# Optimization experiments

Measured on AMD Instinct MI355X. Metric: run time of the kernel, lower is better.

The kernel has to match this reference:

```python
import math
import jax, jax.numpy as jnp
import numpy as np

B, FIN, FOUT, M = 8192, 512, 512, 8
INV_SQRT_2PI = 1.0 / math.sqrt(2.0 * math.pi)
SQRT_HALF = math.sqrt(0.5)


def setup_inputs() -> dict:
    key = jax.random.key(0)
    k = jax.random.split(key, 7)
    x = jax.random.normal(k[0], (B, FIN), dtype=jnp.float32)
    nan_mask = jax.random.uniform(k[1], (B, FIN)) < 0.15
    nan_mask = nan_mask.at[:, 0].set(True)  # every row has >=1 NaN -> GMM path taken, den > 0
    x = jnp.where(nan_mask, jnp.nan, x)
    bound = 1.0 / math.sqrt(FIN)  # torch nn.Linear default init range
    W = jax.random.uniform(k[2], (FOUT, FIN), dtype=jnp.float32, minval=-bound, maxval=bound)
    b = jax.random.uniform(k[3], (FOUT,), dtype=jnp.float32, minval=-bound, maxval=bound)
    mean_p = 0.1 * jax.random.normal(k[4], (M, FIN), dtype=jnp.float32)
    log_std2 = 0.1 * jax.random.normal(k[5], (M, FIN), dtype=jnp.float32)
    log_weights = jax.random.normal(k[6], (M,), dtype=jnp.float32)
    return {"x": x, "W": W, "b": b, "mean_p": mean_p,
            "log_std2": log_std2, "log_weights": log_weights}


def _nr(z):
    # pdf(z) + z * Phi(z), the Gaussian 'nr' function from the paper
    pdf = INV_SQRT_2PI * jnp.exp(-0.5 * z * z)
    return pdf + z * 0.5 * (1.0 + jax.lax.erf(z * SQRT_HALF))


def reference(x, W, b, mean_p, log_std2, log_weights):
    nan = jnp.isnan(x)                         # [B, FIN]
    empty = jnp.any(nan, axis=-1)[:, None]     # [B, 1]
    mask = nan[:, None, :]                     # [B, 1, FIN]
    # impute NaNs with per-mode GMM means
    mean = jnp.where(mask, mean_p, x[:, None, :])                   # [B, M, FIN]
    num = jnp.einsum('bmf,of->bom', mean, W) + b[None, :, None]     # [B, FOUT, M]
    std2 = jnp.where(mask, jnp.exp(log_std2), jnp.float32(0.0))     # [B, M, FIN]
    den = jnp.sqrt(jnp.einsum('bmf,of->bom', std2, W * W))          # [B, FOUT, M]
    nr = den * _nr(num / (den + 1e-9))                              # [B, FOUT, M]
    mixture = nr @ jax.nn.softmax(log_weights)                      # [B, FOUT]
    return jnp.where(empty, mixture, jax.nn.relu(num[..., 0]))
```

## Files before the change

kernel.cpp:

```cpp
#include <hip/hip_runtime.h>
#include <math.h>

typedef __attribute__((ext_vector_type(8))) short short8;
typedef __attribute__((ext_vector_type(8))) _Float16 f16x8;
typedef __attribute__((ext_vector_type(4))) float floatx4;
typedef __attribute__((ext_vector_type(4))) int intx4;
typedef __attribute__((ext_vector_type(16))) int intx16;

#define B_ROWS 8192
#define FIN    512
#define FOUT   512
#define QS     4096.0f
#define QINV   0.000244140625f

#define WSB_SW   0UL
#define WSB_CNT  64UL
#define WSB_BASE 65536UL
#define WSB_XCH  16842752UL
#define WSB_MSK  25231360UL
#define WSB_WH   33619968UL
#define WSB_BCT  34144256UL

__device__ __forceinline__ void gl2lds16(const void* g, void* l) {
    __builtin_amdgcn_global_load_lds((const __attribute__((address_space(1))) void*)g,
                                     (__attribute__((address_space(3))) void*)l,
                                     16, 0, 0);
}

__device__ __forceinline__ float frcp(float x) { float r; asm("v_rcp_f32 %0, %1" : "=v"(r) : "v"(x)); return r; }
__device__ __forceinline__ float frsq(float x) { float r; asm("v_rsq_f32 %0, %1" : "=v"(r) : "v"(x)); return r; }
__device__ __forceinline__ float fexp2(float x){ float r; asm("v_exp_f32 %0, %1" : "=v"(r) : "v"(x)); return r; }

__global__ __launch_bounds__(256) void prep_all(const float* __restrict__ W,
                                                const float* __restrict__ mean_p,
                                                const float* __restrict__ ls2,
                                                const float* __restrict__ x,
                                                const float* __restrict__ lw,
                                                signed char* __restrict__ bct,
                                                _Float16* __restrict__ Wh,
                                                _Float16* __restrict__ xch,
                                                signed char* __restrict__ msk,
                                                int* __restrict__ cnts,
                                                float* __restrict__ wsf) {
    int tid = threadIdx.x, lane = tid & 63, wid = tid >> 6;
    if (blockIdx.x < 2048) {
        int n  = blockIdx.x * 4 + wid;
        int fc = lane << 3;
        int o = n >> 4, t = n & 15;
        const float* wp = W + (size_t)o * FIN + fc;
        float v[8];
        if (t < 8) {
            const float* mp = mean_p + (size_t)t * FIN + fc;
#pragma unroll
            for (int j = 0; j < 8; ++j) v[j] = mp[j] * wp[j];
            if (t == 0) {
                f16x8 wv;
#pragma unroll
                for (int j = 0; j < 8; ++j) wv[j] = (_Float16)wp[j];
                *(f16x8*)(Wh + (size_t)o * FIN + fc) = wv;
            }
        } else {
            const float* lp = ls2 + (size_t)(t - 8) * FIN + fc;
#pragma unroll
            for (int j = 0; j < 8; ++j) v[j] = expf(lp[j]) * wp[j] * wp[j];
        }
        unsigned long long pack = 0;
#pragma unroll
        for (int j = 0; j < 8; ++j) {
            int q = (int)rintf(v[j] * QS);
            q = q > 127 ? 127 : (q < -127 ? -127 : q);
            pack |= ((unsigned long long)(unsigned char)(signed char)q) << (8 * j);
        }
        *(unsigned long long*)(bct + (size_t)n * FIN + fc) = pack;
    } else {
        int row = (blockIdx.x - 2048) * 4 + wid;
        const float* xr = x + (size_t)row * FIN + lane * 8;
        float4 a = *(const float4*)xr;
        float4 b = *(const float4*)(xr + 4);
        float v[8] = {a.x, a.y, a.z, a.w, b.x, b.y, b.z, b.w};
        f16x8 xo;
        unsigned long long mpack = 0;
        bool anyn = false;
#pragma unroll
        for (int j = 0; j < 8; ++j) {
            bool isn = (v[j] != v[j]);
            anyn |= isn;
            xo[j] = (_Float16)(isn ? 0.f : v[j]);
            mpack |= ((unsigned long long)(isn ? 1u : 0u)) << (8 * j);
        }
        *(f16x8*)(xch + (size_t)row * FIN + lane * 8) = xo;
        *(unsigned long long*)(msk + (size_t)row * FIN + lane * 8) = mpack;
        bool any = __any(anyn);
        if (lane == 0) cnts[row] = any ? 1 : 0;
        if (blockIdx.x == 2048 && tid == 0) {
            float mx = lw[0];
            for (int m = 1; m < 8; ++m) mx = fmaxf(mx, lw[m]);
            float e[8]; float s = 0.f;
            for (int m = 0; m < 8; ++m) { e[m] = expf(lw[m] - mx); s += e[m]; }
            for (int m = 0; m < 8; ++m) wsf[m] = e[m] / s;
        }
    }
}

__global__ __launch_bounds__(256) void gemm_base(const _Float16* __restrict__ xch,
                                                 const _Float16* __restrict__ Wh,
                                                 _Float16* __restrict__ base) {
    __shared__ short As[128 * 64];
    __shared__ short Bs[64 * 64];
    int tid = threadIdx.x, lane = tid & 63, wid = tid >> 6;
    int wr = wid >> 1, wc = wid & 1;
    int bb0 = blockIdx.y * 128;
    int ob0 = blockIdx.x * 64;

    floatx4 acc[4][2];
#pragma unroll
    for (int mi = 0; mi < 4; ++mi)
#pragma unroll
        for (int ni = 0; ni < 2; ++ni) acc[mi][ni] = (floatx4){0.f, 0.f, 0.f, 0.f};

    for (int ks = 0; ks < FIN; ks += 64) {
        __syncthreads();
#pragma unroll
        for (int i = 0; i < 4; ++i) {
            int cid = i * 256 + tid, row = cid >> 3, c = cid & 7;
            short8 v = *(const short8*)((const short*)xch + (((size_t)(bb0 + row)) << 9) + ks + c * 8);
            *(short8*)(&As[row * 64 + ((c ^ (row & 7)) << 3)]) = v;
        }
#pragma unroll
        for (int i = 0; i < 2; ++i) {
            int cid = i * 256 + tid, row = cid >> 3, c = cid & 7;
            short8 v = *(const short8*)((const short*)Wh + (((size_t)(ob0 + row)) << 9) + ks + c * 8);
            *(short8*)(&Bs[row * 64 + ((c ^ (row & 7)) << 3)]) = v;
        }
        __syncthreads();
#pragma unroll
        for (int kk = 0; kk < 2; ++kk) {
            f16x8 av[4], bv[2];
#pragma unroll
            for (int mi = 0; mi < 4; ++mi) {
                int row = wr * 64 + mi * 16 + (lane & 15);
                int c = kk * 4 + (lane >> 4);
                av[mi] = *(const f16x8*)(&As[row * 64 + ((c ^ (row & 7)) << 3)]);
            }
#pragma unroll
            for (int ni = 0; ni < 2; ++ni) {
                int row = wc * 32 + ni * 16 + (lane & 15);
                int c = kk * 4 + (lane >> 4);
                bv[ni] = *(const f16x8*)(&Bs[row * 64 + ((c ^ (row & 7)) << 3)]);
            }
#pragma unroll
            for (int mi = 0; mi < 4; ++mi)
#pragma unroll
                for (int ni = 0; ni < 2; ++ni)
                    acc[mi][ni] = __builtin_amdgcn_mfma_f32_16x16x32_f16(av[mi], bv[ni], acc[mi][ni], 0, 0, 0);
        }
    }
#pragma unroll
    for (int mi = 0; mi < 4; ++mi)
#pragma unroll
        for (int ni = 0; ni < 2; ++ni)
#pragma unroll
            for (int r = 0; r < 4; ++r) {
                int row = bb0 + wr * 64 + mi * 16 + (lane >> 4) * 4 + r;
                int col = ob0 + wc * 32 + ni * 16 + (lane & 15);
                base[(size_t)row * FOUT + col] = (_Float16)acc[mi][ni][r];
            }
}

__global__ __launch_bounds__(512, 4) void gmm_fused(const signed char* __restrict__ msk,
                                                    const signed char* __restrict__ bct,
                                                    const float* __restrict__ wsf,
                                                    const int* __restrict__ cnts,
                                                    const _Float16* __restrict__ baseh,
                                                    const float* __restrict__ bias,
                                                    float* __restrict__ out) {
    __shared__ char lds[73728];

    int tid = threadIdx.x, lane = tid & 63, wid = tid >> 6;
    int wr = wid >> 1, wc = wid & 1;

    int id = blockIdx.x, gid = id >> 6, wi = id & 63;
    int my = (gid >> 3) * 8 + (wi >> 3);
    int nx = (gid & 7) * 8 + (wi & 7);
    int b0 = my * 256, n0 = nx * 128;

    const char* mB = (const char*)msk;
    const char* bB = (const char*)bct;

    int rA0 = (wid + 0) * 16 + (lane >> 2);
    int rA1 = (wid + 8) * 16 + (lane >> 2);
    int rB0 = rA0;
    const char* gA0 = mB + (size_t)(b0 + rA0) * 512 + (((lane & 3) ^ ((rA0 >> 1) & 3)) << 4);
    const char* gA1 = mB + (size_t)(b0 + rA1) * 512 + (((lane & 3) ^ ((rA1 >> 1) & 3)) << 4);
    const char* gB0 = bB + (size_t)(n0 + rB0) * 512 + (((lane & 3) ^ ((rB0 >> 1) & 3)) << 4);
    const int lA0o = (wid + 0) * 1024;
    const int lA1o = (wid + 8) * 1024;
    const int lB0o = 16384 + wid * 1024;

    int offA[2], offB[2];
#pragma unroll
    for (int mi = 0; mi < 2; ++mi) {
        int r = wr * 64 + mi * 32 + (lane & 31);
        offA[mi] = r * 64 + ((((lane >> 5) ^ ((r >> 1) & 3))) << 4);
    }
#pragma unroll
    for (int ni = 0; ni < 2; ++ni) {
        int r = wc * 64 + ni * 32 + (lane & 31);
        offB[ni] = 16384 + r * 64 + ((((lane >> 5) ^ ((r >> 1) & 3))) << 4);
    }

    intx16 acc[2][2];
#pragma unroll
    for (int mi = 0; mi < 2; ++mi)
#pragma unroll
        for (int ni = 0; ni < 2; ++ni)
#pragma unroll
            for (int e = 0; e < 16; ++e) acc[mi][ni][e] = 0;

#define STAGE(T)                                             \
    {                                                        \
        const int bo_ = ((T) % 3) * 24576;                   \
        gl2lds16(gA0 + (T) * 64, lds + bo_ + lA0o);          \
        gl2lds16(gA1 + (T) * 64, lds + bo_ + lA1o);          \
        gl2lds16(gB0 + (T) * 64, lds + bo_ + lB0o);          \
    }

    STAGE(0); STAGE(1);

#pragma unroll
    for (int t = 0; t < 8; ++t) {
        if (t < 7) asm volatile("s_waitcnt vmcnt(3)" ::: "memory");
        else       asm volatile("s_waitcnt vmcnt(0)" ::: "memory");
        __builtin_amdgcn_s_barrier();
        asm volatile("" ::: "memory");
        if (t + 2 < 8) STAGE(t + 2);

        const int bo = (t % 3) * 24576;
#pragma unroll
        for (int kk = 0; kk < 2; ++kk) {
            const int kx = kk << 5;
            intx4 av[2], bv[2];
#pragma unroll
            for (int mi = 0; mi < 2; ++mi) av[mi] = *(const intx4*)(lds + bo + (offA[mi] ^ kx));
#pragma unroll
            for (int ni = 0; ni < 2; ++ni) bv[ni] = *(const intx4*)(lds + bo + (offB[ni] ^ kx));
            __builtin_amdgcn_s_setprio(1);
#pragma unroll
            for (int mi = 0; mi < 2; ++mi)
#pragma unroll
                for (int ni = 0; ni < 2; ++ni)
                    acc[mi][ni] = __builtin_amdgcn_mfma_i32_32x32x32_i8(av[mi], bv[ni], acc[mi][ni], 0, 0, 0);
            __builtin_amdgcn_s_setprio(0);
        }
    }
#undef STAGE

    __syncthreads();

    float swv[8];
#pragma unroll
    for (int m = 0; m < 8; ++m) swv[m] = wsf[m];

    int* sci = (int*)lds + wid * 1056;
    int cl = lane & 31, oh = lane >> 5;

#pragma unroll
    for (int mi = 0; mi < 2; ++mi) {
#pragma unroll
        for (int ni = 0; ni < 2; ++ni) {
#pragma unroll
            for (int reg = 0; reg < 16; ++reg) {
                int r = (reg & 3) + 8 * (reg >> 2) + 4 * oh;
                sci[r * 33 + cl] = acc[mi][ni][reg];
            }
            __asm__ volatile("s_waitcnt lgkmcnt(0)" ::: "memory");

            float cn[8], cd[8];
#pragma unroll
            for (int tt = 0; tt < 8; ++tt) cn[tt] = (float)sci[cl * 33 + oh * 16 + tt] * QINV;
#pragma unroll
            for (int tt = 0; tt < 8; ++tt) cd[tt] = (float)sci[cl * 33 + oh * 16 + 8 + tt] * QINV;

            int b = b0 + wr * 64 + mi * 32 + cl;
            int o = ((n0 + wc * 64 + ni * 32) >> 4) + oh;
            float basev = (float)baseh[(size_t)b * FOUT + o];
            float K0 = basev + bias[o];
            bool empty = cnts[b] > 0;

            float mix = 0.f, num0 = 0.f;
#pragma unroll
            for (int m = 0; m < 8; ++m) {
                float num = K0 + cn[m];
                if (m == 0) num0 = num;
                float rs  = frsq(fmaxf(cd[m], 1e-20f));
                float den = cd[m] * rs;
                float z   = num * rs;
                float az  = fabsf(z);
                float E   = fexp2((z * z) * -0.72134752044448170f);
                float t1  = frcp(fmaf(0.2316419f, az, 1.0f));
                float h   = fmaf(t1, 0.5307027145f, -0.7265760135f);
                h = fmaf(t1, h, 0.7107068705f);
                h = fmaf(t1, h, -0.142248368f);
                h = fmaf(t1, h, 0.127414796f);
                float u   = t1 * h;
                float v   = fmaf(-az, u, 0.3989422804014327f);
                float g   = fmaf(E, v, fmaxf(z, 0.f));
                mix = fmaf(swv[m], den * g, mix);
            }
            out[(size_t)b * FOUT + o] = empty ? mix : fmaxf(num0, 0.f);
        }
    }
}

extern "C" void kernel_launch(void* const* d_in, const int* in_sizes, int n_in,
                              void* d_out, int out_size, void* d_ws, size_t ws_size,
                              hipStream_t stream) {
    const float* x        = (const float*)d_in[0];
    const float* W        = (const float*)d_in[1];
    const float* bvec     = (const float*)d_in[2];
    const float* mean_p   = (const float*)d_in[3];
    const float* log_std2 = (const float*)d_in[4];
    const float* lw       = (const float*)d_in[5];
    float* out = (float*)d_out;

    char* wsb = (char*)d_ws;
    float*        wsf  = (float*)wsb;
    int*          cnts = (int*)(wsb + WSB_CNT);
    _Float16*     base = (_Float16*)(wsb + WSB_BASE);
    _Float16*     xch  = (_Float16*)(wsb + WSB_XCH);
    signed char*  msk  = (signed char*)(wsb + WSB_MSK);
    _Float16*     Wh   = (_Float16*)(wsb + WSB_WH);
    signed char*  bct  = (signed char*)(wsb + WSB_BCT);

    prep_all<<<4096, 256, 0, stream>>>(W, mean_p, log_std2, x, lw, bct, Wh, xch, msk, cnts, wsf);
    gemm_base<<<dim3(FOUT / 64, B_ROWS / 128), 256, 0, stream>>>(xch, Wh, base);
    gmm_fused<<<(B_ROWS / 256) * (8192 / 128), 512, 0, stream>>>(msk, bct, wsf, cnts, base, bvec, out);
}
```

Before: 79.52 us.

## Pipeline base GEMM with async LDS loads; retile GMM kernel to 256 threads

The fp16 base GEMM now uses direct global-to-LDS loads into a triple-buffered pipeline with prefetch depth two, replacing synchronous register-staged loads. The int8 GMM kernel drops to 256 threads per block, each wave holding 4x2 MFMA tiles. Base, bias and count values are preloaded into registers before the main loop, and the block-to-tile swizzle is changed. Variance coefficients get a separate, finer quantization scale for better precision, and expf becomes a raw exp2 instruction. Larger per-wave tiles raise register pressure and may lower occupancy.

Measured after the change: 83.57 us. 5.1% more time.

```diff
diff --git a/kernel.cpp b/kernel.cpp
--- a/kernel.cpp
+++ b/kernel.cpp
@@ -10,8 +10,10 @@
 #define B_ROWS 8192
 #define FIN    512
 #define FOUT   512
-#define QS     4096.0f
-#define QINV   0.000244140625f
+#define QSN    4096.0f
+#define QINVN  0.000244140625f
+#define QSD    32768.0f
+#define QINVD  0.000030517578125f
 
 #define WSB_SW   0UL
 #define WSB_CNT  64UL
@@ -49,10 +51,12 @@
         int o = n >> 4, t = n & 15;
         const float* wp = W + (size_t)o * FIN + fc;
         float v[8];
+        float qs;
         if (t < 8) {
             const float* mp = mean_p + (size_t)t * FIN + fc;
 #pragma unroll
             for (int j = 0; j < 8; ++j) v[j] = mp[j] * wp[j];
+            qs = QSN;
             if (t == 0) {
                 f16x8 wv;
 #pragma unroll
@@ -62,12 +66,13 @@
         } else {
             const float* lp = ls2 + (size_t)(t - 8) * FIN + fc;
 #pragma unroll
-            for (int j = 0; j < 8; ++j) v[j] = expf(lp[j]) * wp[j] * wp[j];
+            for (int j = 0; j < 8; ++j) v[j] = fexp2(lp[j] * 1.4426950408889634f) * wp[j] * wp[j];
+            qs = QSD;
         }
         unsigned long long pack = 0;
 #pragma unroll
         for (int j = 0; j < 8; ++j) {
-            int q = (int)rintf(v[j] * QS);
+            int q = (int)rintf(v[j] * qs);
             q = q > 127 ? 127 : (q < -127 ? -127 : q);
             pack |= ((unsigned long long)(unsigned char)(signed char)q) << (8 * j);
         }
@@ -102,59 +107,91 @@
     }
 }
 
-__global__ __launch_bounds__(256) void gemm_base(const _Float16* __restrict__ xch,
-                                                 const _Float16* __restrict__ Wh,
-                                                 _Float16* __restrict__ base) {
-    __shared__ short As[128 * 64];
-    __shared__ short Bs[64 * 64];
+__global__ __launch_bounds__(256, 2) void gemm_base(const _Float16* __restrict__ xch,
+                                                    const _Float16* __restrict__ Wh,
+                                                    _Float16* __restrict__ base) {
+    __shared__ char lds[73728];
     int tid = threadIdx.x, lane = tid & 63, wid = tid >> 6;
     int wr = wid >> 1, wc = wid & 1;
     int bb0 = blockIdx.y * 128;
     int ob0 = blockIdx.x * 64;
 
+    const char* xB = (const char*)xch;
+    const char* wB = (const char*)Wh;
+
+    int rA0 = (wid +  0) * 8 + (lane >> 3);
+    int rA1 = (wid +  4) * 8 + (lane >> 3);
+    int rA2 = (wid +  8) * 8 + (lane >> 3);
+    int rA3 = (wid + 12) * 8 + (lane >> 3);
+    const char* gA0 = xB + (size_t)(bb0 + rA0) * 1024 + (((lane & 7) ^ (rA0 & 7)) << 4);
+    const char* gA1 = xB + (size_t)(bb0 + rA1) * 1024 + (((lane & 7) ^ (rA1 & 7)) << 4);
+    const char* gA2 = xB + (size_t)(bb0 + rA2) * 1024 + (((lane & 7) ^ (rA2 & 7)) << 4);
+    const char* gA3 = xB + (size_t)(bb0 + rA3) * 1024 + (((lane & 7) ^ (rA3 & 7)) << 4);
+    const char* gB0 = wB + (size_t)(ob0 + rA0) * 1024 + (((lane & 7) ^ (rA0 & 7)) << 4);
+    const char* gB1 = wB + (size_t)(ob0 + rA1) * 1024 + (((lane & 7) ^ (rA1 & 7)) << 4);
+    const int lA0o = (wid +  0) * 1024, lA1o = (wid +  4) * 1024;
+    const int lA2o = (wid +  8) * 1024, lA3o = (wid + 12) * 1024;
+    const int lB0o = 16384 + (wid + 0) * 1024, lB1o = 16384 + (wid + 4) * 1024;
+
+    int offA[4], offB[2];
+#pragma unroll
+    for (int mi = 0; mi < 4; ++mi) {
+        int r = wr * 64 + mi * 16 + (lane & 15);
+        offA[mi] = r * 128 + ((((lane >> 4) ^ (r & 7))) << 4);
+    }
+#pragma unroll
+    for (int ni = 0; ni < 2; ++ni) {
+        int r = wc * 32 + ni * 16 + (lane & 15);
+        offB[ni] = 16384 + r * 128 + ((((lane >> 4) ^ (r & 7))) << 4);
+    }
+
     floatx4 acc[4][2];
 #pragma unroll
     for (int mi = 0; mi < 4; ++mi)
 #pragma unroll
         for (int ni = 0; ni < 2; ++ni) acc[mi][ni] = (floatx4){0.f, 0.f, 0.f, 0.f};
 
-    for (int ks = 0; ks < FIN; ks += 64) {
-        __syncthreads();
-#pragma unroll
-        for (int i = 0; i < 4; ++i) {
-            int cid = i * 256 + tid, row = cid >> 3, c = cid & 7;
-            short8 v = *(const short8*)((const short*)xch + (((size_t)(bb0 + row)) << 9) + ks + c * 8);
-            *(short8*)(&As[row * 64 + ((c ^ (row & 7)) << 3)]) = v;
-        }
-#pragma unroll
-        for (int i = 0; i < 2; ++i) {
-            int cid = i * 256 + tid, row = cid >> 3, c = cid & 7;
-            short8 v = *(const short8*)((const short*)Wh + (((size_t)(ob0 + row)) << 9) + ks + c * 8);
-            *(short8*)(&Bs[row * 64 + ((c ^ (row & 7)) << 3)]) = v;
-        }
-        __syncthreads();
+#define STAGEB(T)                                            \
+    {                                                        \
+        const int bo_ = ((T) % 3) * 24576;                   \
+        gl2lds16(gA0 + (T) * 128, lds + bo_ + lA0o);         \
+        gl2lds16(gA1 + (T) * 128, lds + bo_ + lA1o);         \
+        gl2lds16(gA2 + (T) * 128, lds + bo_ + lA2o);         \
+        gl2lds16(gA3 + (T) * 128, lds + bo_ + lA3o);         \
+        gl2lds16(gB0 + (T) * 128, lds + bo_ + lB0o);         \
+        gl2lds16(gB1 + (T) * 128, lds + bo_ + lB1o);         \
+    }
+
+    STAGEB(0); STAGEB(1);
+
+#pragma unroll
+    for (int t = 0; t < 8; ++t) {
+        if (t < 7) asm volatile("s_waitcnt vmcnt(6)" ::: "memory");
+        else       asm volatile("s_waitcnt vmcnt(0)" ::: "memory");
+        __builtin_amdgcn_s_barrier();
+        asm volatile("" ::: "memory");
+        if (t + 2 < 8) STAGEB(t + 2);
+
+        const int bo = (t % 3) * 24576;
 #pragma unroll
         for (int kk = 0; kk < 2; ++kk) {
+            const int kx = kk << 6;
             f16x8 av[4], bv[2];
 #pragma unroll
-            for (int mi = 0; mi < 4; ++mi) {
-                int row = wr * 64 + mi * 16 + (lane & 15);
-                int c = kk * 4 + (lane >> 4);
-                av[mi] = *(const f16x8*)(&As[row * 64 + ((c ^ (row & 7)) << 3)]);
-            }
-#pragma unroll
-            for (int ni = 0; ni < 2; ++ni) {
-                int row = wc * 32 + ni * 16 + (lane & 15);
-                int c = kk * 4 + (lane >> 4);
-                bv[ni] = *(const f16x8*)(&Bs[row * 64 + ((c ^ (row & 7)) << 3)]);
-            }
+            for (int mi = 0; mi < 4; ++mi) av[mi] = *(const f16x8*)(lds + bo + (offA[mi] ^ kx));
+#pragma unroll
+            for (int ni = 0; ni < 2; ++ni) bv[ni] = *(const f16x8*)(lds + bo + (offB[ni] ^ kx));
+            __builtin_amdgcn_s_setprio(1);
 #pragma unroll
             for (int mi = 0; mi < 4; ++mi)
 #pragma unroll
                 for (int ni = 0; ni < 2; ++ni)
                     acc[mi][ni] = __builtin_amdgcn_mfma_f32_16x16x32_f16(av[mi], bv[ni], acc[mi][ni], 0, 0, 0);
-        }
-    }
+            __builtin_amdgcn_s_setprio(0);
+        }
+    }
+#undef STAGEB
+
 #pragma unroll
     for (int mi = 0; mi < 4; ++mi)
 #pragma unroll
@@ -163,11 +200,11 @@
             for (int r = 0; r < 4; ++r) {
                 int row = bb0 + wr * 64 + mi * 16 + (lane >> 4) * 4 + r;
                 int col = ob0 + wc * 32 + ni * 16 + (lane & 15);
-                base[(size_t)row * FOUT + col] = (_Float16)acc[mi][ni][r];
+                base[((size_t)row << 9) + col] = (_Float16)acc[mi][ni][r];
             }
 }
 
-__global__ __launch_bounds__(512, 4) void gmm_fused(const signed char* __restrict__ msk,
+__global__ __launch_bounds__(256, 2) void gmm_fused(const signed char* __restrict__ msk,
                                                     const signed char* __restrict__ bct,
                                                     const float* __restrict__ wsf,
                                                     const int* __restrict__ cnts,
@@ -179,28 +216,47 @@
     int tid = threadIdx.x, lane = tid & 63, wid = tid >> 6;
     int wr = wid >> 1, wc = wid & 1;
 
-    int id = blockIdx.x, gid = id >> 6, wi = id & 63;
-    int my = (gid >> 3) * 8 + (wi >> 3);
-    int nx = (gid & 7) * 8 + (wi & 7);
+    int id = blockIdx.x, g = id >> 8, wi = id & 255;
+    int my = (g >> 2) * 16 + (wi >> 4);
+    int nx = (g & 3) * 16 + (wi & 15);
     int b0 = my * 256, n0 = nx * 128;
 
     const char* mB = (const char*)msk;
     const char* bB = (const char*)bct;
 
-    int rA0 = (wid + 0) * 16 + (lane >> 2);
-    int rA1 = (wid + 8) * 16 + (lane >> 2);
-    int rB0 = rA0;
+    int cl = lane & 31, oh = lane >> 5;
+    _Float16 base_r[4][2];
+    float bias_r[2];
+    int cnt_r[4];
+#pragma unroll
+    for (int ni = 0; ni < 2; ++ni) bias_r[ni] = bias[nx * 8 + wc * 4 + ni * 2 + oh];
+#pragma unroll
+    for (int mi = 0; mi < 4; ++mi) {
+        int b = b0 + wr * 128 + mi * 32 + cl;
+        cnt_r[mi] = cnts[b];
+#pragma unroll
+        for (int ni = 0; ni < 2; ++ni)
+            base_r[mi][ni] = baseh[((size_t)b << 9) + nx * 8 + wc * 4 + ni * 2 + oh];
+    }
+
+    int rA0 = (wid +  0) * 16 + (lane >> 2);
+    int rA1 = (wid +  4) * 16 + (lane >> 2);
+    int rA2 = (wid +  8) * 16 + (lane >> 2);
+    int rA3 = (wid + 12) * 16 + (lane >> 2);
     const char* gA0 = mB + (size_t)(b0 + rA0) * 512 + (((lane & 3) ^ ((rA0 >> 1) & 3)) << 4);
     const char* gA1 = mB + (size_t)(b0 + rA1) * 512 + (((lane & 3) ^ ((rA1 >> 1) & 3)) << 4);
-    const char* gB0 = bB + (size_t)(n0 + rB0) * 512 + (((lane & 3) ^ ((rB0 >> 1) & 3)) << 4);
-    const int lA0o = (wid + 0) * 1024;
-    const int lA1o = (wid + 8) * 1024;
-    const int lB0o = 16384 + wid * 1024;
-
-    int offA[2], offB[2];
-#pragma unroll
-    for (int mi = 0; mi < 2; ++mi) {
-        int r = wr * 64 + mi * 32 + (lane & 31);
+    const char* gA2 = mB + (size_t)(b0 + rA2) * 512 + (((lane & 3) ^ ((rA2 >> 1) & 3)) << 4);
+    const char* gA3 = mB + (size_t)(b0 + rA3) * 512 + (((lane & 3) ^ ((rA3 >> 1) & 3)) << 4);
+    const char* gB0 = bB + (size_t)(n0 + rA0) * 512 + (((lane & 3) ^ ((rA0 >> 1) & 3)) << 4);
+    const char* gB1 = bB + (size_t)(n0 + rA1) * 512 + (((lane & 3) ^ ((rA1 >> 1) & 3)) << 4);
+    const int lA0o = (wid +  0) * 1024, lA1o = (wid +  4) * 1024;
+    const int lA2o = (wid +  8) * 1024, lA3o = (wid + 12) * 1024;
+    const int lB0o = 16384 + (wid + 0) * 1024, lB1o = 16384 + (wid + 4) * 1024;
+
+    int offA[4], offB[2];
+#pragma unroll
+    for (int mi = 0; mi < 4; ++mi) {
+        int r = wr * 128 + mi * 32 + (lane & 31);
         offA[mi] = r * 64 + ((((lane >> 5) ^ ((r >> 1) & 3))) << 4);
     }
 #pragma unroll
@@ -209,9 +265,9 @@
         offB[ni] = 16384 + r * 64 + ((((lane >> 5) ^ ((r >> 1) & 3))) << 4);
     }
 
-    intx16 acc[2][2];
-#pragma unroll
-    for (int mi = 0; mi < 2; ++mi)
+    intx16 acc[4][2];
+#pragma unroll
+    for (int mi = 0; mi < 4; ++mi)
 #pragma unroll
         for (int ni = 0; ni < 2; ++ni)
 #pragma unroll
@@ -222,14 +278,17 @@
         const int bo_ = ((T) % 3) * 24576;                   \
         gl2lds16(gA0 + (T) * 64, lds + bo_ + lA0o);          \
         gl2lds16(gA1 + (T) * 64, lds + bo_ + lA1o);          \
+        gl2lds16(gA2 + (T) * 64, lds + bo_ + lA2o);          \
+        gl2lds16(gA3 + (T) * 64, lds + bo_ + lA3o);          \
         gl2lds16(gB0 + (T) * 64, lds + bo_ + lB0o);          \
+        gl2lds16(gB1 + (T) * 64, lds + bo_ + lB1o);          \
     }
 
     STAGE(0); STAGE(1);
 
 #pragma unroll
     for (int t = 0; t < 8; ++t) {
-        if (t < 7) asm volatile("s_waitcnt vmcnt(3)" ::: "memory");
+        if (t < 7) asm volatile("s_waitcnt vmcnt(6)" ::: "memory");
         else       asm volatile("s_waitcnt vmcnt(0)" ::: "memory");
         __builtin_amdgcn_s_barrier();
         asm volatile("" ::: "memory");
@@ -239,14 +298,14 @@
 #pragma unroll
         for (int kk = 0; kk < 2; ++kk) {
             const int kx = kk << 5;
-            intx4 av[2], bv[2];
-#pragma unroll
-            for (int mi = 0; mi < 2; ++mi) av[mi] = *(const intx4*)(lds + bo + (offA[mi] ^ kx));
+            intx4 av[4], bv[2];
+#pragma unroll
+            for (int mi = 0; mi < 4; ++mi) av[mi] = *(const intx4*)(lds + bo + (offA[mi] ^ kx));
 #pragma unroll
             for (int ni = 0; ni < 2; ++ni) bv[ni] = *(const intx4*)(lds + bo + (offB[ni] ^ kx));
             __builtin_amdgcn_s_setprio(1);
 #pragma unroll
-            for (int mi = 0; mi < 2; ++mi)
+            for (int mi = 0; mi < 4; ++mi)
 #pragma unroll
                 for (int ni = 0; ni < 2; ++ni)
                     acc[mi][ni] = __builtin_amdgcn_mfma_i32_32x32x32_i8(av[mi], bv[ni], acc[mi][ni], 0, 0, 0);
@@ -262,10 +321,9 @@
     for (int m = 0; m < 8; ++m) swv[m] = wsf[m];
 
     int* sci = (int*)lds + wid * 1056;
-    int cl = lane & 31, oh = lane >> 5;
-
-#pragma unroll
-    for (int mi = 0; mi < 2; ++mi) {
+
+#pragma unroll
+    for (int mi = 0; mi < 4; ++mi) {
 #pragma unroll
         for (int ni = 0; ni < 2; ++ni) {
 #pragma unroll
@@ -277,15 +335,14 @@
 
             float cn[8], cd[8];
 #pragma unroll
-            for (int tt = 0; tt < 8; ++tt) cn[tt] = (float)sci[cl * 33 + oh * 16 + tt] * QINV;
-#pragma unroll
-            for (int tt = 0; tt < 8; ++tt) cd[tt] = (float)sci[cl * 33 + oh * 16 + 8 + tt] * QINV;
-
-            int b = b0 + wr * 64 + mi * 32 + cl;
-            int o = ((n0 + wc * 64 + ni * 32) >> 4) + oh;
-            float basev = (float)baseh[(size_t)b * FOUT + o];
-            float K0 = basev + bias[o];
-            bool empty = cnts[b] > 0;
+            for (int tt = 0; tt < 8; ++tt) cn[tt] = (float)sci[cl * 33 + oh * 16 + tt] * QINVN;
+#pragma unroll
+            for (int tt = 0; tt < 8; ++tt) cd[tt] = (float)sci[cl * 33 + oh * 16 + 8 + tt] * QINVD;
+
+            int b = b0 + wr * 128 + mi * 32 + cl;
+            int o = nx * 8 + wc * 4 + ni * 2 + oh;
+            float K0 = (float)base_r[mi][ni] + bias_r[ni];
+            bool empty = cnt_r[mi] > 0;
 
             float mix = 0.f, num0 = 0.f;
 #pragma unroll
@@ -304,10 +361,10 @@
                 h = fmaf(t1, h, 0.127414796f);
                 float u   = t1 * h;
                 float v   = fmaf(-az, u, 0.3989422804014327f);
-                float g   = fmaf(E, v, fmaxf(z, 0.f));
-                mix = fmaf(swv[m], den * g, mix);
+                float gg  = fmaf(E, v, fmaxf(z, 0.f));
+                mix = fmaf(swv[m], den * gg, mix);
             }
-            out[(size_t)b * FOUT + o] = empty ? mix : fmaxf(num0, 0.f);
+            out[((size_t)b << 9) + o] = empty ? mix : fmaxf(num0, 0.f);
         }
     }
 }
@@ -334,5 +391,5 @@
 
     prep_all<<<4096, 256, 0, stream>>>(W, mean_p, log_std2, x, lw, bct, Wh, xch, msk, cnts, wsf);
     gemm_base<<<dim3(FOUT / 64, B_ROWS / 128), 256, 0, stream>>>(xch, Wh, base);
-    gmm_fused<<<(B_ROWS / 256) * (8192 / 128), 512, 0, stream>>>(msk, bct, wsf, cnts, base, bvec, out);
-}
+    gmm_fused<<<(B_ROWS / 256) * (8192 / 128), 256, 0, stream>>>(msk, bct, wsf, cnts, base, bvec, out);
+}
```
